# Performance work log

Hardware: AMD Instinct MI355X
Metric: run time of the kernel (lower is better)

## Reference

```python
import math
import jax, jax.numpy as jnp
import numpy as np

HEADS = 4
BOTTLENECK = 8

def setup_inputs() -> dict:
    key = jax.random.key(0)
    ks = jax.random.split(key, 12)
    B, N, H, k = 8, 10000, 512, BOTTLENECK
    hd = H // HEADS
    s = 1.0 / math.sqrt(H)
    return {
        "x": jax.random.normal(ks[0], (B, N, H), dtype=jnp.float32),
        "Wq": jax.random.uniform(ks[1], (H, H), jnp.float32, -s, s),
        "bq": jnp.zeros((H,), jnp.float32),
        "Wk": jax.random.uniform(ks[2], (H, H), jnp.float32, -s, s),
        "bk": jnp.zeros((H,), jnp.float32),
        "Wv": jax.random.uniform(ks[3], (H, H), jnp.float32, -s, s),
        "bv": jnp.zeros((H,), jnp.float32),
        "E": jax.random.normal(ks[4], (HEADS, N, k), jnp.float32) / math.sqrt(k),
        "Fp": jax.random.normal(ks[5], (HEADS, N, k), jnp.float32) / math.sqrt(k),
        "gbu": jax.random.normal(ks[6], (HEADS, k, k), jnp.float32) * 0.1,
        "gbv": jax.random.normal(ks[7], (HEADS, k, k), jnp.float32) * 0.1,
        "Wo": jax.random.uniform(ks[8], (H, H), jnp.float32, -s, s),
        "bo": jnp.zeros((H,), jnp.float32),
        "log_reg": jnp.asarray(math.log(1e-5), jnp.float32),
    }

def reference(x, Wq, bq, Wk, bk, Wv, bv, E, Fp, gbu, gbv, Wo, bo, log_reg):
    B, N, H = x.shape
    hd = H // HEADS
    def split_heads(t):
        return t.reshape(B, N, HEADS, hd).transpose(0, 2, 1, 3)  # [B,h,N,hd]
    q = split_heads(x @ Wq.T + bq)
    k = split_heads(x @ Wk.T + bk)
    v = split_heads(x @ Wv.T + bv)
    # Faithful to torch einsum 'hik,bhnd->bhkd' (i and n summed independently)
    k_proj = jnp.einsum('hik,bhnd->bhkd', E, k)   # [B,h,k,hd]
    v_proj = jnp.einsum('hik,bhnd->bhkd', Fp, v)  # [B,h,k,hd]
    scores = jnp.einsum('bhnd,bhkd->bhnk', q, k_proj) / math.sqrt(hd)
    graph_bias = gbu @ gbv                                  # [h,k,k]
    bias_diag = jnp.diagonal(graph_bias, axis1=1, axis2=2)  # [h,k]
    scores = scores + bias_diag[None, :, None, :]
    attn = jax.nn.softmax(scores, axis=-1)
    out = jnp.einsum('bhnk,bhkd->bhnd', attn, v_proj)
    out = out.transpose(0, 2, 1, 3).reshape(B, N, H)
    out = out @ Wo.T + bo
    reg = jnp.exp(log_reg) * (jnp.mean(jnp.abs(attn)) + jnp.mean(jnp.abs(graph_bias)) * 0.1)
    return out, reg
```

## Files before the change

### kernel.cpp

```cpp
#include <hip/hip_runtime.h>
#include <math.h>

#define HEADS 4
#define KB 8
#define Bsz 8
#define Nn 10000
#define Hh 512
#define HD 128
#define NPART 64

#define XS_OFF   0
#define KSUM_OFF 4096
#define VSUM_OFF 8192
#define WQE_OFF  12288
#define WOE_OFF  28672
#define ESUM_OFF 45056
#define FSUM_OFF 45088
#define BQ_OFF   45120
#define BD_OFF   45152


__global__ __launch_bounds__(256) void k_part(const float* __restrict__ x,
                                              const float* __restrict__ E,
                                              const float* __restrict__ Fp,
                                              float* __restrict__ xpart,
                                              float* __restrict__ efpart) {
    int blk = blockIdx.x;
    int t = threadIdx.x;
    if (blk < NPART * Bsz) {
        int p = blk >> 3, b = blk & 7;
        const int CH = (Nn + NPART - 1) / NPART;
        int n0 = p * CH, n1 = min(n0 + CH, Nn);
        int c = t * 2;
        float a0 = 0.f, a1 = 0.f;
        const float* base = x + (size_t)b * Nn * Hh + c;
#pragma unroll 4
        for (int n = n0; n < n1; ++n) {
            float2 v = *(const float2*)(base + (size_t)n * Hh);
            a0 += v.x; a1 += v.y;
        }
        float* o = xpart + (size_t)(p * Bsz + b) * Hh;
        o[c] = a0; o[c + 1] = a1;
    } else {
        int idx = blk - NPART * Bsz;
        int src = idx >> 5, h = (idx >> 3) & 3, ch = idx & 7;
        const float* S = src ? Fp : E;
        const int CHE = Nn / 8;
        int n0 = ch * CHE, n1 = n0 + CHE;
        int kk = t & 7, part = t >> 3;
        float acc = 0.f;
        const float* base = S + (size_t)h * Nn * KB;
#pragma unroll 4
        for (int n = n0 + part; n < n1; n += 32) acc += base[n * KB + kk];
        __shared__ float sd[256];
        sd[t] = acc;
        __syncthreads();
        for (int s = 128; s >= 8; s >>= 1) {
            if (t < s) sd[t] += sd[t + s];
            __syncthreads();
        }
        if (t < 8) efpart[idx * 8 + t] = sd[t];
    }
}

__global__ __launch_bounds__(256) void k_reduce(const float* __restrict__ xpart,
                                                const float* __restrict__ efpart,
                                                float* __restrict__ xs,
                                                float* __restrict__ esum,
                                                float* __restrict__ fsum) {
    int blk = blockIdx.x, t = threadIdx.x;
    if (blk < 16) {
        int o = blk * 256 + t;
        float a = 0.f;
#pragma unroll 8
        for (int p = 0; p < NPART; ++p) a += xpart[(size_t)p * (Bsz * Hh) + o];
        xs[o] = a;
    } else if (t < 64) {
        int src = t >> 5, rem = t & 31;
        float a = 0.f;
#pragma unroll
        for (int ch = 0; ch < 8; ++ch)
            a += efpart[((src * 4 + (rem >> 3)) * 8 + ch) * 8 + (rem & 7)];
        if (src == 0) esum[rem] = a; else fsum[rem] = a;
    }
}

__global__ __launch_bounds__(256) void k_gemv(const float* __restrict__ Wk,
                                              const float* __restrict__ bk,
                                              const float* __restrict__ Wv,
                                              const float* __restrict__ bv,
                                              const float* __restrict__ xs,
                                              float* __restrict__ ksum,
                                              float* __restrict__ vsum) {
    int m = blockIdx.x;
    int rg = blockIdx.y;
    const float* W = m ? Wv : Wk;
    const float* bias = m ? bv : bk;
    float* out = m ? vsum : ksum;
    __shared__ float xsL[Bsz * Hh];
    int t = threadIdx.x;
    for (int i = t; i < Bsz * Hh; i += 256) xsL[i] = xs[i];
    __syncthreads();
    int wid = t >> 6, lane = t & 63;
    for (int i = 0; i < 16; ++i) {
        int r = rg * 64 + wid + 4 * i;
        float4 wa = *(const float4*)(W + (size_t)r * Hh + lane * 4);
        float4 wb = *(const float4*)(W + (size_t)r * Hh + 256 + lane * 4);
        float p[Bsz];
#pragma unroll
        for (int b = 0; b < Bsz; ++b) {
            const float4 x0 = *(const float4*)(&xsL[b * Hh + lane * 4]);
            const float4 x1 = *(const float4*)(&xsL[b * Hh + 256 + lane * 4]);
            p[b] = wa.x * x0.x + wa.y * x0.y + wa.z * x0.z + wa.w * x0.w +
                   wb.x * x1.x + wb.y * x1.y + wb.z * x1.z + wb.w * x1.w;
        }
#pragma unroll
        for (int off = 32; off >= 1; off >>= 1)
#pragma unroll
            for (int b = 0; b < Bsz; ++b) p[b] += __shfl_xor(p[b], off, 64);
        if (lane == 0) {
            float bb = (float)Nn * bias[r];
#pragma unroll
            for (int b = 0; b < Bsz; ++b) out[b * Hh + r] = p[b] + bb;
        }
    }
}

__global__ __launch_bounds__(256) void k_eff2(const float* __restrict__ Wq,
                                              const float* __restrict__ Wo,
                                              const float* __restrict__ ksum,
                                              const float* __restrict__ vsum,
                                              float* __restrict__ wqe,
                                              float* __restrict__ woe,
                                              const float* __restrict__ bq,
                                              const float* __restrict__ gbu,
                                              const float* __restrict__ gbv,
                                              const float* __restrict__ log_reg,
                                              float* __restrict__ bias_q,
                                              float* __restrict__ bias_diag,
                                              float* __restrict__ reg_out) {
    int blk = blockIdx.x;
    int t = threadIdx.x;
    __shared__ float sL[256];
    if (blk < 64) {
        int b = blk >> 3, rem = blk & 7, h = rem >> 1, m = rem & 1;
        const float* s = (m ? vsum : ksum) + b * Hh + h * HD;
        float* out = (m ? woe : wqe) + (size_t)(b * HEADS + h) * Hh;
        if (t < HD) sL[t] = s[t];
        __syncthreads();
        float a0 = 0.f, a1 = 0.f;
        if (m == 0) {
            const float* Wb = Wq + (size_t)h * HD * Hh;
#pragma unroll 4
            for (int d = 0; d < HD; ++d) {
                float sv = sL[d];
                a0 += Wb[(size_t)d * Hh + t] * sv;
                a1 += Wb[(size_t)d * Hh + t + 256] * sv;
            }
        } else {
            const float* W0 = Wo + (size_t)t * Hh + h * HD;
            const float* W1 = Wo + (size_t)(t + 256) * Hh + h * HD;
            for (int d = 0; d < HD; d += 4) {
                a0 += W0[d] * sL[d] + W0[d + 1] * sL[d + 1] + W0[d + 2] * sL[d + 2] + W0[d + 3] * sL[d + 3];
                a1 += W1[d] * sL[d] + W1[d + 1] * sL[d + 1] + W1[d + 2] * sL[d + 2] + W1[d + 3] * sL[d + 3];
            }
        }
        out[t] = a0;
        out[t + 256] = a1;
    } else {
        int h = t >> 6, i = (t >> 3) & 7, j = t & 7;
        float gb = 0.f;
#pragma unroll
        for (int l = 0; l < 8; ++l) gb += gbu[h * 64 + i * 8 + l] * gbv[h * 64 + l * 8 + j];
        if (i == j) bias_diag[h * 8 + i] = gb;
        sL[t] = fabsf(gb);
        __syncthreads();
        for (int s = 128; s >= 1; s >>= 1) {
            if (t < s) sL[t] += sL[t + s];
            __syncthreads();
        }
        if (t == 0) {
            float gbmean = sL[0] / 256.f;
            reg_out[0] = expf(log_reg[0]) * (0.125f + gbmean * 0.1f);
        }
        if (t < 32) {
            int b = t >> 2, hh = t & 3;
            float a = 0.f;
            for (int d = 0; d < HD; ++d) a += bq[hh * HD + d] * ksum[b * Hh + hh * HD + d];
            bias_q[t] = a;
        }
    }
}

__global__ __launch_bounds__(256) void k_main(const float* __restrict__ x,
                                              const float* __restrict__ bo,
                                              const float* __restrict__ wqe,
                                              const float* __restrict__ woe,
                                              const float* __restrict__ esum,
                                              const float* __restrict__ fsum,
                                              const float* __restrict__ bias_q,
                                              const float* __restrict__ bias_diag,
                                              float* __restrict__ out) {
    int b = blockIdx.y;
    __shared__ float woL[HEADS * Hh];
    int t = threadIdx.x;
    const float* woe_b = woe + (size_t)b * HEADS * Hh;
    for (int i = t; i < HEADS * Hh; i += 256) woL[i] = woe_b[i];

    int wid = t >> 6, lane = t & 63;
    const float* wqe_b = wqe + (size_t)b * HEADS * Hh;
    float4 wqa[HEADS], wqb[HEADS];
#pragma unroll
    for (int h = 0; h < HEADS; ++h) {
        wqa[h] = *(const float4*)(wqe_b + h * Hh + lane * 4);
        wqb[h] = *(const float4*)(wqe_b + h * Hh + 256 + lane * 4);
    }
    float4 boa = *(const float4*)(bo + lane * 4);
    float4 bob = *(const float4*)(bo + 256 + lane * 4);
    int j = lane & 31, g = j >> 3;
    float eV = esum[j];
    float fV = fsum[j];
    float bdV = bias_diag[j];
    float bqV = bias_q[b * HEADS + g];
    __syncthreads();

    const float inv_sqrt_hd = 0.08838834764831843f;
    int wavesPerB = gridDim.x * 4;

    for (int n = blockIdx.x * 4 + wid; n < Nn; n += wavesPerB) {
        const float* xr = x + ((size_t)b * Nn + n) * Hh;
        float4 xa = *(const float4*)(xr + lane * 4);
        float4 xb = *(const float4*)(xr + 256 + lane * 4);
        float p[HEADS];
#pragma unroll
        for (int h = 0; h < HEADS; ++h) {
            p[h] = xa.x * wqa[h].x + xa.y * wqa[h].y + xa.z * wqa[h].z + xa.w * wqa[h].w +
                   xb.x * wqb[h].x + xb.y * wqb[h].y + xb.z * wqb[h].z + xb.w * wqb[h].w;
        }
#pragma unroll
        for (int off = 32; off >= 1; off >>= 1)
#pragma unroll
            for (int h = 0; h < HEADS; ++h) p[h] += __shfl_xor(p[h], off, 64);

        float sq = (p[g] + bqV) * inv_sqrt_hd;
        float sc = eV * sq + bdV;
        float m = sc;
        m = fmaxf(m, __shfl_xor(m, 1, 64));
        m = fmaxf(m, __shfl_xor(m, 2, 64));
        m = fmaxf(m, __shfl_xor(m, 4, 64));
        float e = __expf(sc - m);
        float se = e, sw = e * fV;
        se += __shfl_xor(se, 1, 64); sw += __shfl_xor(sw, 1, 64);
        se += __shfl_xor(se, 2, 64); sw += __shfl_xor(sw, 2, 64);
        se += __shfl_xor(se, 4, 64); sw += __shfl_xor(sw, 4, 64);
        float wv = sw / se;
        float w0 = __shfl(wv, 0, 64);
        float w1 = __shfl(wv, 8, 64);
        float w2 = __shfl(wv, 16, 64);
        float w3 = __shfl(wv, 24, 64);

        float4 oa = boa, ob = bob;
        {
            float4 wa = *(const float4*)(&woL[0 * Hh + lane * 4]);
            float4 wb = *(const float4*)(&woL[0 * Hh + 256 + lane * 4]);
            oa.x += w0 * wa.x; oa.y += w0 * wa.y; oa.z += w0 * wa.z; oa.w += w0 * wa.w;
            ob.x += w0 * wb.x; ob.y += w0 * wb.y; ob.z += w0 * wb.z; ob.w += w0 * wb.w;
        }
        {
            float4 wa = *(const float4*)(&woL[1 * Hh + lane * 4]);
            float4 wb = *(const float4*)(&woL[1 * Hh + 256 + lane * 4]);
            oa.x += w1 * wa.x; oa.y += w1 * wa.y; oa.z += w1 * wa.z; oa.w += w1 * wa.w;
            ob.x += w1 * wb.x; ob.y += w1 * wb.y; ob.z += w1 * wb.z; ob.w += w1 * wb.w;
        }
        {
            float4 wa = *(const float4*)(&woL[2 * Hh + lane * 4]);
            float4 wb = *(const float4*)(&woL[2 * Hh + 256 + lane * 4]);
            oa.x += w2 * wa.x; oa.y += w2 * wa.y; oa.z += w2 * wa.z; oa.w += w2 * wa.w;
            ob.x += w2 * wb.x; ob.y += w2 * wb.y; ob.z += w2 * wb.z; ob.w += w2 * wb.w;
        }
        {
            float4 wa = *(const float4*)(&woL[3 * Hh + lane * 4]);
            float4 wb = *(const float4*)(&woL[3 * Hh + 256 + lane * 4]);
            oa.x += w3 * wa.x; oa.y += w3 * wa.y; oa.z += w3 * wa.z; oa.w += w3 * wa.w;
            ob.x += w3 * wb.x; ob.y += w3 * wb.y; ob.z += w3 * wb.z; ob.w += w3 * wb.w;
        }
        float* orow = out + ((size_t)b * Nn + n) * Hh;
        *(float4*)(orow + lane * 4) = oa;
        *(float4*)(orow + 256 + lane * 4) = ob;
    }
}

extern "C" void kernel_launch(void* const* d_in, const int* in_sizes, int n_in,
                              void* d_out, int out_size, void* d_ws, size_t ws_size,
                              hipStream_t stream) {
    const float* x       = (const float*)d_in[0];
    const float* Wq      = (const float*)d_in[1];
    const float* bq      = (const float*)d_in[2];
    const float* Wk      = (const float*)d_in[3];
    const float* bk      = (const float*)d_in[4];
    const float* Wv      = (const float*)d_in[5];
    const float* bv      = (const float*)d_in[6];
    const float* E       = (const float*)d_in[7];
    const float* Fp      = (const float*)d_in[8];
    const float* gbu     = (const float*)d_in[9];
    const float* gbv     = (const float*)d_in[10];
    const float* Wo      = (const float*)d_in[11];
    const float* bo      = (const float*)d_in[12];
    const float* log_reg = (const float*)d_in[13];

    float* out = (float*)d_out;
    float* ws = (float*)d_ws;
    float* xs   = ws + XS_OFF;
    float* ksum = ws + KSUM_OFF;
    float* vsum = ws + VSUM_OFF;
    float* wqe  = ws + WQE_OFF;
    float* woe  = ws + WOE_OFF;
    float* esum = ws + ESUM_OFF;
    float* fsum = ws + FSUM_OFF;
    float* bias_q = ws + BQ_OFF;
    float* bias_diag = ws + BD_OFF;
    float* reg_out = out + (size_t)Bsz * Nn * Hh;

    float* xpart  = out;
    float* efpart = out + (size_t)NPART * Bsz * Hh;

    k_part<<<NPART * Bsz + 64, 256, 0, stream>>>(x, E, Fp, xpart, efpart);
    k_reduce<<<17, 256, 0, stream>>>(xpart, efpart, xs, esum, fsum);
    k_gemv<<<dim3(2, 8), 256, 0, stream>>>(Wk, bk, Wv, bv, xs, ksum, vsum);
    k_eff2<<<65, 256, 0, stream>>>(Wq, Wo, ksum, vsum, wqe, woe,
                                   bq, gbu, gbv, log_reg, bias_q, bias_diag, reg_out);
    k_main<<<dim3(250, Bsz), 256, 0, stream>>>(x, bo, wqe, woe, esum, fsum, bias_q, bias_diag, out);
}
```

Before: 385.7 us.

## Keep output weights in registers and use a transpose-style butterfly reduction

```diff
diff --git a/kernel.cpp b/kernel.cpp
--- a/kernel.cpp
+++ b/kernel.cpp
@@ -9,7 +9,6 @@
 #define HD 128
 #define NPART 64
 
-#define XS_OFF   0
 #define KSUM_OFF 4096
 #define VSUM_OFF 8192
 #define WQE_OFF  12288
@@ -202,30 +201,34 @@
                                               const float* __restrict__ bias_diag,
                                               float* __restrict__ out) {
     int b = blockIdx.y;
-    __shared__ float woL[HEADS * Hh];
     int t = threadIdx.x;
+    int wid = t >> 6, lane = t & 63;
+
+    const float* wqe_b = wqe + (size_t)b * HEADS * Hh;
     const float* woe_b = woe + (size_t)b * HEADS * Hh;
-    for (int i = t; i < HEADS * Hh; i += 256) woL[i] = woe_b[i];
-
-    int wid = t >> 6, lane = t & 63;
-    const float* wqe_b = wqe + (size_t)b * HEADS * Hh;
-    float4 wqa[HEADS], wqb[HEADS];
+    float4 wqa[HEADS], wqb[HEADS], woa[HEADS], wob[HEADS];
 #pragma unroll
     for (int h = 0; h < HEADS; ++h) {
         wqa[h] = *(const float4*)(wqe_b + h * Hh + lane * 4);
         wqb[h] = *(const float4*)(wqe_b + h * Hh + 256 + lane * 4);
+        woa[h] = *(const float4*)(woe_b + h * Hh + lane * 4);
+        wob[h] = *(const float4*)(woe_b + h * Hh + 256 + lane * 4);
     }
     float4 boa = *(const float4*)(bo + lane * 4);
     float4 bob = *(const float4*)(bo + 256 + lane * 4);
-    int j = lane & 31, g = j >> 3;
-    float eV = esum[j];
-    float fV = fsum[j];
-    float bdV = bias_diag[j];
-    float bqV = bias_q[b * HEADS + g];
-    __syncthreads();
+
+    int q = lane >> 4;
+    int hq = (q == 0) ? 0 : (q == 1) ? 2 : (q == 2) ? 1 : 3;
+    int kk = lane & 7;
+    float eV = esum[hq * KB + kk];
+    float fV = fsum[hq * KB + kk];
+    float bdV = bias_diag[hq * KB + kk];
+    float bqV = bias_q[b * HEADS + hq];
 
     const float inv_sqrt_hd = 0.08838834764831843f;
     int wavesPerB = gridDim.x * 4;
+    bool hi32 = (lane & 32) != 0;
+    bool hi16 = (lane & 16) != 0;
 
     for (int n = blockIdx.x * 4 + wid; n < Nn; n += wavesPerB) {
         const float* xr = x + ((size_t)b * Nn + n) * Hh;
@@ -237,12 +240,21 @@
             p[h] = xa.x * wqa[h].x + xa.y * wqa[h].y + xa.z * wqa[h].z + xa.w * wqa[h].w +
                    xb.x * wqb[h].x + xb.y * wqb[h].y + xb.z * wqb[h].z + xb.w * wqb[h].w;
         }
-#pragma unroll
-        for (int off = 32; off >= 1; off >>= 1)
-#pragma unroll
-            for (int h = 0; h < HEADS; ++h) p[h] += __shfl_xor(p[h], off, 64);
-
-        float sq = (p[g] + bqV) * inv_sqrt_hd;
+        float A  = hi32 ? p[1] : p[0];
+        float Bv = hi32 ? p[0] : p[1];
+        A += __shfl_xor(Bv, 32, 64);
+        float C  = hi32 ? p[3] : p[2];
+        float D  = hi32 ? p[2] : p[3];
+        C += __shfl_xor(D, 32, 64);
+        float Ev = hi16 ? C : A;
+        float Fv = hi16 ? A : C;
+        Ev += __shfl_xor(Fv, 16, 64);
+        Ev += __shfl_xor(Ev, 1, 64);
+        Ev += __shfl_xor(Ev, 2, 64);
+        Ev += __shfl_xor(Ev, 4, 64);
+        Ev += __shfl_xor(Ev, 8, 64);
+
+        float sq = (Ev + bqV) * inv_sqrt_hd;
         float sc = eV * sq + bdV;
         float m = sc;
         m = fmaxf(m, __shfl_xor(m, 1, 64));
@@ -255,35 +267,20 @@
         se += __shfl_xor(se, 4, 64); sw += __shfl_xor(sw, 4, 64);
         float wv = sw / se;
         float w0 = __shfl(wv, 0, 64);
-        float w1 = __shfl(wv, 8, 64);
         float w2 = __shfl(wv, 16, 64);
-        float w3 = __shfl(wv, 24, 64);
+        float w1 = __shfl(wv, 32, 64);
+        float w3 = __shfl(wv, 48, 64);
 
         float4 oa = boa, ob = bob;
-        {
-            float4 wa = *(const float4*)(&woL[0 * Hh + lane * 4]);
-            float4 wb = *(const float4*)(&woL[0 * Hh + 256 + lane * 4]);
-            oa.x += w0 * wa.x; oa.y += w0 * wa.y; oa.z += w0 * wa.z; oa.w += w0 * wa.w;
-            ob.x += w0 * wb.x; ob.y += w0 * wb.y; ob.z += w0 * wb.z; ob.w += w0 * wb.w;
-        }
-        {
-            float4 wa = *(const float4*)(&woL[1 * Hh + lane * 4]);
-            float4 wb = *(const float4*)(&woL[1 * Hh + 256 + lane * 4]);
-            oa.x += w1 * wa.x; oa.y += w1 * wa.y; oa.z += w1 * wa.z; oa.w += w1 * wa.w;
-            ob.x += w1 * wb.x; ob.y += w1 * wb.y; ob.z += w1 * wb.z; ob.w += w1 * wb.w;
-        }
-        {
-            float4 wa = *(const float4*)(&woL[2 * Hh + lane * 4]);
-            float4 wb = *(const float4*)(&woL[2 * Hh + 256 + lane * 4]);
-            oa.x += w2 * wa.x; oa.y += w2 * wa.y; oa.z += w2 * wa.z; oa.w += w2 * wa.w;
-            ob.x += w2 * wb.x; ob.y += w2 * wb.y; ob.z += w2 * wb.z; ob.w += w2 * wb.w;
-        }
-        {
-            float4 wa = *(const float4*)(&woL[3 * Hh + lane * 4]);
-            float4 wb = *(const float4*)(&woL[3 * Hh + 256 + lane * 4]);
-            oa.x += w3 * wa.x; oa.y += w3 * wa.y; oa.z += w3 * wa.z; oa.w += w3 * wa.w;
-            ob.x += w3 * wb.x; ob.y += w3 * wb.y; ob.z += w3 * wb.z; ob.w += w3 * wb.w;
-        }
+        oa.x += w0 * woa[0].x + w1 * woa[1].x + w2 * woa[2].x + w3 * woa[3].x;
+        oa.y += w0 * woa[0].y + w1 * woa[1].y + w2 * woa[2].y + w3 * woa[3].y;
+        oa.z += w0 * woa[0].z + w1 * woa[1].z + w2 * woa[2].z + w3 * woa[3].z;
+        oa.w += w0 * woa[0].w + w1 * woa[1].w + w2 * woa[2].w + w3 * woa[3].w;
+        ob.x += w0 * wob[0].x + w1 * wob[1].x + w2 * wob[2].x + w3 * wob[3].x;
+        ob.y += w0 * wob[0].y + w1 * wob[1].y + w2 * wob[2].y + w3 * wob[3].y;
+        ob.z += w0 * wob[0].z + w1 * wob[1].z + w2 * wob[2].z + w3 * wob[3].z;
+        ob.w += w0 * wob[0].w + w1 * wob[1].w + w2 * wob[2].w + w3 * wob[3].w;
+
         float* orow = out + ((size_t)b * Nn + n) * Hh;
         *(float4*)(orow + lane * 4) = oa;
         *(float4*)(orow + 256 + lane * 4) = ob;
@@ -310,7 +307,7 @@
 
     float* out = (float*)d_out;
     float* ws = (float*)d_ws;
-    float* xs   = ws + XS_OFF;
+    float* xs   = ws;
     float* ksum = ws + KSUM_OFF;
     float* vsum = ws + VSUM_OFF;
     float* wqe  = ws + WQE_OFF;
```

Result: no change. 382.2 us (-0.9%).
